# Performance work log

Measured on AMD Instinct MI355X. Metric: run time of the kernel, lower is better.

## Reference

```python
import jax, jax.numpy as jnp
import numpy as np
import math

D_MODEL = 1024
N_HEADS = 16
D_HEAD = D_MODEL // N_HEADS


def setup_inputs() -> dict:
    key = jax.random.key(0)
    ks = jax.random.split(key, 9)
    B, S = 4, 2048
    scale = 1.0 / math.sqrt(D_MODEL)
    x = jax.random.normal(ks[0], (B, S, D_MODEL), dtype=jnp.float32)
    # nn.Linear weights stored as [out, in]; we keep [in, out] for x @ W
    w_q = jax.random.uniform(ks[1], (D_MODEL, D_MODEL), jnp.float32, -scale, scale)
    b_q = jax.random.uniform(ks[2], (D_MODEL,), jnp.float32, -scale, scale)
    w_k = jax.random.uniform(ks[3], (D_MODEL, D_MODEL), jnp.float32, -scale, scale)
    b_k = jax.random.uniform(ks[4], (D_MODEL,), jnp.float32, -scale, scale)
    w_v = jax.random.uniform(ks[5], (D_MODEL, D_MODEL), jnp.float32, -scale, scale)
    b_v = jax.random.uniform(ks[6], (D_MODEL,), jnp.float32, -scale, scale)
    w_o = jax.random.uniform(ks[7], (D_MODEL, D_MODEL), jnp.float32, -scale, scale)
    b_o = jax.random.uniform(ks[8], (D_MODEL,), jnp.float32, -scale, scale)
    return {"x": x, "w_q": w_q, "b_q": b_q, "w_k": w_k, "b_k": b_k,
            "w_v": w_v, "b_v": b_v, "w_o": w_o, "b_o": b_o}


def reference(x, w_q, b_q, w_k, b_k, w_v, b_v, w_o, b_o):
    B, S, _ = x.shape
    def split_heads(t):  # [B,S,D] -> [B,H,S,Dh]
        return t.reshape(B, S, N_HEADS, D_HEAD).transpose(0, 2, 1, 3)
    q = split_heads(x @ w_q + b_q)
    k = split_heads(x @ w_k + b_k)
    v = split_heads(x @ w_v + b_v)
    scores = jnp.einsum('bhqd,bhkd->bhqk', q, k) / math.sqrt(D_HEAD)
    attn = jax.nn.softmax(scores, axis=-1)  # dropout p=0 -> identity
    ctx = jnp.einsum('bhqk,bhkd->bhqd', attn, v)
    ctx = ctx.transpose(0, 2, 1, 3).reshape(B, S, D_MODEL)
    return ctx @ w_o + b_o
```

## Files before the change

### kernel.cpp

```cpp
#include <hip/hip_runtime.h>
#include <hip/hip_bf16.h>

#define DM   1024
#define SEQ  2048
#define NH   16
#define DH   64
#define BH   64
#define MTOT 8192

typedef __attribute__((ext_vector_type(8)))  short short8;
typedef __attribute__((ext_vector_type(4)))  short short4v;
typedef __attribute__((ext_vector_type(4)))  float f32x4;
typedef __attribute__((ext_vector_type(2)))  float f32x2;
typedef __attribute__((ext_vector_type(16))) float f32x16;
typedef __attribute__((ext_vector_type(4)))  float fvec4;
typedef __attribute__((ext_vector_type(4)))  int   i32x4;
typedef unsigned short ushort_t;

#define AS1 __attribute__((address_space(1)))
#define AS3 __attribute__((address_space(3)))

#define QSCALE 0.18033688011112042f

static __device__ __forceinline__ unsigned short f2bf(float f){
  __bf16 h = (__bf16)f;
  return __builtin_bit_cast(unsigned short, h);
}

static __device__ __forceinline__ float fexp2(float x){
  float r;
  asm("v_exp_f32 %0, %1" : "=v"(r) : "v"(x));
  return r;
}

static __device__ __forceinline__ f32x2 pkadd(f32x2 a, f32x2 b){
  f32x2 d;
  asm("v_pk_add_f32 %0, %1, %2" : "=v"(d) : "v"(a), "v"(b));
  return d;
}

static __device__ __forceinline__ void gld16(const void* g, void* l){
  __builtin_amdgcn_global_load_lds((const AS1 int*)g, (AS3 int*)l, 16, 0, 0);
}

__global__ void k_cast_x(const float* __restrict__ x, ushort_t* __restrict__ xb){
  const size_t i = (size_t)blockIdx.x*256 + threadIdx.x;
  const fvec4* xv = (const fvec4*)x;
  fvec4 a = xv[2*i], b = xv[2*i+1];
  short8 r;
  #pragma unroll
  for (int j=0;j<4;++j) r[j]   = (short)f2bf(a[j]);
  #pragma unroll
  for (int j=0;j<4;++j) r[4+j] = (short)f2bf(b[j]);
  ((short8*)xb)[i] = r;
}

__global__ void k_cast_wt(const float* __restrict__ wq, const float* __restrict__ wk,
                          const float* __restrict__ wv, const float* __restrict__ wo,
                          ushort_t* __restrict__ wt){
  const int z = blockIdx.y;
  const float* W = (z==0)?wq:(z==1)?wk:(z==2)?wv:wo;
  ushort_t* Wt = wt + (size_t)z*DM*DM;
  const int k0 = (blockIdx.x & 15)*64, n0 = (blockIdx.x >> 4)*64;
  __shared__ float tile[64][65];
  const int t = threadIdx.x;
  #pragma unroll
  for (int it=0; it<4; ++it){
    int c = it*256 + t;
    int rr = c>>4, cc = c&15;
    fvec4 v = *(const fvec4*)(W + (size_t)(k0+rr)*DM + n0 + cc*4);
    #pragma unroll
    for (int j=0;j<4;++j) tile[cc*4+j][rr] = v[j];
  }
  __syncthreads();
  #pragma unroll
  for (int it=0; it<4; ++it){
    int c = it*256 + t;
    int nn = c>>4, kk = c&15;
    short4v r;
    #pragma unroll
    for (int j=0;j<4;++j) r[j] = (short)f2bf(tile[nn][kk*4+j]);
    *(short4v*)(Wt + (size_t)(n0+nn)*DM + k0 + kk*4) = r;
  }
}

template<int MODE>
__global__ __launch_bounds__(256, 2)
void k_gemm128(const ushort_t* __restrict__ A, const ushort_t* __restrict__ WtBase,
               const float* __restrict__ b0, const float* __restrict__ b1,
               const float* __restrict__ b2,
               ushort_t* __restrict__ obf, float* __restrict__ of32){
  const int by = blockIdx.y;
  const int z  = (MODE==0) ? (by>>3) : 0;
  const int n0 = (MODE==0) ? ((by&7)*128) : by*128;
  const ushort_t* Wt = WtBase + (size_t)z*DM*DM;
  const float* bias = (z==0)? b0 : (z==1? b1 : b2);
  __shared__ ushort_t Al[128*32];
  __shared__ ushort_t Bl[128*32];
  const int t = threadIdx.x;
  const int wid = t>>6, l = t&63, g = l>>4, li = l&15;
  const int m0 = blockIdx.x*128;
  const int wr = (wid>>1)*64, wc = (wid&1)*64;
  const int srow = t>>2, schunk = (t&3)*8;

  f32x4 acc[4][4] = {};

  for (int kt = 0; kt < DM; kt += 32){
    __syncthreads();
    #pragma unroll
    for (int c = 0; c < 2; ++c){
      gld16(A  + (size_t)(m0 + c*64 + srow)*DM + kt + schunk, (char*)Al + c*4096 + wid*1024);
      gld16(Wt + (size_t)(n0 + c*64 + srow)*DM + kt + schunk, (char*)Bl + c*4096 + wid*1024);
    }
    __syncthreads();
    short8 af[4], bw[4];
    #pragma unroll
    for (int mt=0; mt<4; ++mt)
      af[mt] = *(const short8*)(Al + (wr + mt*16 + li)*32 + g*8);
    #pragma unroll
    for (int nt=0; nt<4; ++nt)
      bw[nt] = *(const short8*)(Bl + (wc + nt*16 + li)*32 + g*8);
    #pragma unroll
    for (int mt=0; mt<4; ++mt)
      #pragma unroll
      for (int nt=0; nt<4; ++nt)
        acc[mt][nt] = __builtin_amdgcn_mfma_f32_16x16x32_bf16(af[mt], bw[nt], acc[mt][nt], 0,0,0);
  }

  if constexpr (MODE==0){
    if (z == 2){
      ushort_t* vt = obf + (size_t)2*MTOT*DM;
      #pragma unroll
      for (int nt=0; nt<4; ++nt){
        const int n = n0 + wc + nt*16 + li;
        const float bn = bias[n];
        const int h = n>>6, d = n&63;
        #pragma unroll
        for (int mt=0; mt<4; ++mt){
          const int m = m0 + wr + mt*16 + g*4;
          const int bb = m >> 11, s = m & 2047;
          short4v pk;
          #pragma unroll
          for (int r=0; r<4; ++r) pk[r] = (short)f2bf(acc[mt][nt][r] + bn);
          *(short4v*)(vt + (((size_t)(bb*NH + h)*DH + d)*SEQ + s)) = pk;
        }
      }
    } else {
      const float sc = (z==0) ? QSCALE : 1.f;
      #pragma unroll
      for (int nt=0; nt<4; ++nt){
        const int n = n0 + wc + nt*16 + li;
        const float bn = bias[n];
        #pragma unroll
        for (int mt=0; mt<4; ++mt){
          #pragma unroll
          for (int r=0; r<4; ++r){
            const int m = m0 + wr + mt*16 + g*4 + r;
            const float v = (acc[mt][nt][r] + bn)*sc;
            const int bb = m >> 11, s = m & 2047, h = n >> 6, d = n & 63;
            obf[(size_t)z*MTOT*DM + (((size_t)(bb*NH + h)*SEQ + s)*DH + d)] = f2bf(v);
          }
        }
      }
    }
  } else {
    #pragma unroll
    for (int nt=0; nt<4; ++nt){
      const int n = n0 + wc + nt*16 + li;
      const float bn = bias[n];
      #pragma unroll
      for (int mt=0; mt<4; ++mt){
        #pragma unroll
        for (int r=0; r<4; ++r){
          const int m = m0 + wr + mt*16 + g*4 + r;
          of32[(size_t)m*DM + n] = acc[mt][nt][r] + bn;
        }
      }
    }
  }
}

__global__ __launch_bounds__(256, 3)
void k_attn(const ushort_t* __restrict__ Qb, const ushort_t* __restrict__ Kb,
            const ushort_t* __restrict__ Vtb, ushort_t* __restrict__ ctx){
  const int swz = (blockIdx.x & 7)*128 + (blockIdx.x >> 3);
  const int qb = swz & 15, bh = swz >> 4;
  const int b = bh>>4, h = bh&15;
  const int t = threadIdx.x, wid = t>>6, lane = t&63;
  const int lq = lane&31, hi = lane>>5;
  __shared__ ushort_t Ql[8192];
  __shared__ ushort_t Kl[2][4096];
  __shared__ ushort_t Vl[2][4096];
  const ushort_t* Qh = Qb  + (size_t)bh*SEQ*DH;
  const ushort_t* Kh = Kb  + (size_t)bh*SEQ*DH;
  const ushort_t* Vh = Vtb + (size_t)bh*DH*SEQ;

  #pragma unroll
  for (int i=0; i<2; ++i){
    const int c = wid*2 + i;
    #pragma unroll
    for (int half=0; half<2; ++half)
      gld16(Qh + (size_t)(qb*128 + half*64 + lane)*DH + c*8,
            (char*)Ql + c*2048 + half*1024);
  }

  f32x16 o0 = {}, o1 = {};
  float ls = 0.f;

  #define STAGE(kv0, bi) do {                                              \
    _Pragma("unroll")                                                      \
    for (int i=0; i<2; ++i){                                               \
      const int c = wid*2 + i;                                             \
      gld16(Kh + (size_t)((kv0)+lane)*DH + c*8, (char*)&Kl[bi][0] + c*1024);\
      gld16(Vh + (size_t)lane*SEQ + (kv0) + c*8, (char*)&Vl[bi][0] + c*1024);\
    }                                                                      \
  } while(0)

  STAGE(0, 0);
  __syncthreads();

  const char* Qp = (const char*)Ql + hi*2048 + (wid*32 + lq)*16;

  int cur = 0;
  for (int t64 = 0; t64 < SEQ/64; ++t64){
    if (t64 < SEQ/64 - 1){
      if (cur) STAGE((t64+1)*64, 0); else STAGE((t64+1)*64, 1);
    }
    const char* Kb_ = (const char*)&Kl[cur][0] + hi*1024 + lq*16;
    const char* Vb_ = (const char*)&Vl[cur][0] + hi*1024 + lq*16;

    short8 qf[4];
    #pragma unroll
    for (int ks=0; ks<4; ++ks)
      qf[ks] = *(const short8*)(Qp + ks*4096);

    short8 kf[8];
    #pragma unroll
    for (int ks=0; ks<4; ++ks){
      kf[ks]   = *(const short8*)(Kb_ + ks*2048);
      kf[4+ks] = *(const short8*)(Kb_ + ks*2048 + 512);
    }
    f32x16 s0 = {}, s1 = {};
    __builtin_amdgcn_s_setprio(1);
    #pragma unroll
    for (int ks=0; ks<4; ++ks){
      s0 = __builtin_amdgcn_mfma_f32_32x32x16_bf16(kf[ks],   qf[ks], s0, 0,0,0);
      s1 = __builtin_amdgcn_mfma_f32_32x32x16_bf16(kf[4+ks], qf[ks], s1, 0,0,0);
    }
    __builtin_amdgcn_s_setprio(0);

    #pragma unroll
    for (int r=0; r<16; ++r) s0[r] = fexp2(s0[r]);
    #pragma unroll
    for (int r=0; r<16; ++r) s1[r] = fexp2(s1[r]);
    f32x2 ac = {0.f, 0.f};
    #pragma unroll
    for (int r=0; r<16; r+=4){
      f32x2 u = pkadd(f32x2{s0[r], s0[r+1]}, f32x2{s0[r+2], s0[r+3]});
      f32x2 v = pkadd(f32x2{s1[r], s1[r+1]}, f32x2{s1[r+2], s1[r+3]});
      ac = pkadd(ac, pkadd(u, v));
    }
    ls += ac[0] + ac[1];

    short8 pa[4];
    #pragma unroll
    for (int blk=0; blk<2; ++blk){
      #pragma unroll
      for (int half=0; half<2; ++half){
        i32x4 w;
        #pragma unroll
        for (int wp=0; wp<2; ++wp){
          const int base = half*8 + 2*wp;
          float a0 = blk ? s1[base]   : s0[base];
          float a1 = blk ? s1[base+1] : s0[base+1];
          float c0 = blk ? s1[base+4] : s0[base+4];
          float c1 = blk ? s1[base+5] : s0[base+5];
          int x, y;
          asm("v_cvt_pk_bf16_f32 %0, %1, %2" : "=v"(x) : "v"(a0), "v"(a1));
          asm("v_cvt_pk_bf16_f32 %0, %1, %2" : "=v"(y) : "v"(c0), "v"(c1));
          asm("v_permlane32_swap_b32 %0, %1" : "+v"(x), "+v"(y));
          w[wp] = x; w[2+wp] = y;
        }
        pa[blk*2+half] = __builtin_bit_cast(short8, w);
      }
    }

    short8 vb[8];
    #pragma unroll
    for (int ks=0; ks<4; ++ks){
      vb[ks]   = *(const short8*)(Vb_ + ks*2048);
      vb[4+ks] = *(const short8*)(Vb_ + ks*2048 + 512);
    }
    __builtin_amdgcn_s_setprio(1);
    #pragma unroll
    for (int ks=0; ks<4; ++ks){
      o0 = __builtin_amdgcn_mfma_f32_32x32x16_bf16(pa[ks], vb[ks],   o0, 0,0,0);
      o1 = __builtin_amdgcn_mfma_f32_32x32x16_bf16(pa[ks], vb[4+ks], o1, 0,0,0);
    }
    __builtin_amdgcn_s_setprio(0);

    __syncthreads();
    cur ^= 1;
  }

  ls += __shfl_xor(ls, 32);
  const float inv = 1.f / ls;
  const int qw = qb*128 + wid*32;
  #pragma unroll
  for (int r=0; r<16; ++r){
    const float iv = __shfl(inv, (r&3) + 8*(r>>2) + 4*hi);
    const int qrow = qw + (r&3) + 8*(r>>2) + 4*hi;
    ushort_t* dst = ctx + ((size_t)(b*SEQ + qrow))*DM + h*DH;
    dst[lq]    = f2bf(o0[r]*iv);
    dst[32+lq] = f2bf(o1[r]*iv);
  }
  #undef STAGE
}

extern "C" void kernel_launch(void* const* d_in, const int* in_sizes, int n_in,
                              void* d_out, int out_size, void* d_ws, size_t ws_size,
                              hipStream_t stream){
  const float* x  = (const float*)d_in[0];
  const float* wq = (const float*)d_in[1];
  const float* bq = (const float*)d_in[2];
  const float* wk = (const float*)d_in[3];
  const float* bk = (const float*)d_in[4];
  const float* wv = (const float*)d_in[5];
  const float* bv = (const float*)d_in[6];
  const float* wo = (const float*)d_in[7];
  const float* bo = (const float*)d_in[8];
  float* out = (float*)d_out;

  ushort_t* xb  = (ushort_t*)d_ws;
  ushort_t* wt  = xb  + (size_t)MTOT*DM;
  ushort_t* qkv = wt  + (size_t)4*DM*DM;
  ushort_t* ctx = qkv + (size_t)3*MTOT*DM;

  k_cast_x<<<4096, 256, 0, stream>>>(x, xb);
  k_cast_wt<<<dim3(256,4), 256, 0, stream>>>(wq, wk, wv, wo, wt);
  k_gemm128<0><<<dim3(64,24), 256, 0, stream>>>(xb, wt, bq, bk, bv, qkv, nullptr);
  k_attn<<<1024, 256, 0, stream>>>(qkv, qkv + (size_t)MTOT*DM, qkv + (size_t)2*MTOT*DM, ctx);
  k_gemm128<1><<<dim3(64,8), 256, 0, stream>>>(ctx, wt + (size_t)3*DM*DM, bo, bo, bo, nullptr, out);
}
```

Measured before the change: 279.6 us.

## Replace QKV projection GEMM with double-buffered 256x256-tile kernel

Adds a dedicated QKV projection kernel that uses 256x256 output tiles per 512-thread block. Global-to-LDS loads for the next 64-wide K slice are issued asynchronously into a second 128KB dynamic-shared-memory buffer while MFMAs run on the current one, with explicit waitcnt/barrier staging and raised wave priority around MFMA bursts. This aims to cut the per-K-step load stalls and the extra global traffic of the old 128x128, single-buffered GEMM. The trade-offs are one block per CU because of the large LDS footprint, and a 384-block grid that leaves a partial second wave. The generic GEMM is reduced to the output-projection path only.

```diff
diff --git a/kernel.cpp b/kernel.cpp
--- a/kernel.cpp
+++ b/kernel.cpp
@@ -84,6 +84,139 @@
   }
 }
 
+__global__ __launch_bounds__(512, 2)
+void k_qkv256(const ushort_t* __restrict__ A, const ushort_t* __restrict__ WtBase,
+              const float* __restrict__ bq, const float* __restrict__ bk,
+              const float* __restrict__ bv, ushort_t* __restrict__ qkv){
+  extern __shared__ char smem[];
+  const int t = threadIdx.x, wid = t>>6, lane = t&63;
+  const int g = (lane>>4)&3, li = lane&15;
+  const int wm = wid>>2, wn = wid&3;
+  const int m0 = blockIdx.x*256;
+  const int by = blockIdx.y, z = by>>2, nt0 = (by&3)*256;
+  const ushort_t* Ap = A + (size_t)m0*DM;
+  const ushort_t* Bp = WtBase + (size_t)z*DM*DM + (size_t)nt0*DM;
+  const int irb = wid>>1;
+
+  #define ISSUE(GP, LB, kh, ktt) do{                                        \
+    _Pragma("unroll")                                                       \
+    for (int j=0;j<2;++j){                                                  \
+      const int cg = (kh)*4 + ((wid*2+j)&3);                                \
+      gld16(GP + (size_t)(irb*64 + lane)*DM + (ktt)*64 + cg*8,              \
+            (LB) + cg*4096 + irb*1024);                                     \
+    }                                                                       \
+  }while(0)
+
+  const int aoff = g*4096 + (wm*128 + li)*16;
+  const int boff = g*4096 + (wn*64  + li)*16;
+
+  f32x4 acc[8][4] = {};
+
+  ISSUE(Ap, smem,         0, 0);
+  ISSUE(Bp, smem + 65536, 0, 0);
+  ISSUE(Ap, smem,         1, 0);
+  ISSUE(Bp, smem + 65536, 1, 0);
+  asm volatile("s_waitcnt vmcnt(4)" ::: "memory");
+  __builtin_amdgcn_s_barrier();
+  asm volatile("" ::: "memory");
+
+  #define MFMA16(B0v, B1v, NF0, NF1)                                        \
+    __builtin_amdgcn_s_setprio(1);                                          \
+    _Pragma("unroll")                                                       \
+    for (int mf=0;mf<8;++mf){                                               \
+      acc[mf][NF0] = __builtin_amdgcn_mfma_f32_16x16x32_bf16(a[mf], B0v, acc[mf][NF0], 0,0,0); \
+      acc[mf][NF1] = __builtin_amdgcn_mfma_f32_16x16x32_bf16(a[mf], B1v, acc[mf][NF1], 0,0,0); \
+    }                                                                       \
+    __builtin_amdgcn_s_setprio(0)
+
+  #define BARR() __builtin_amdgcn_s_barrier(); asm volatile("" ::: "memory")
+
+  for (int kt = 0; kt < 16; ++kt){
+    char* curA = smem + (kt&1)*32768;
+    char* curB = smem + 65536 + (kt&1)*32768;
+    char* nxtA = smem + ((kt+1)&1)*32768;
+    char* nxtB = smem + 65536 + ((kt+1)&1)*32768;
+    const bool more = (kt < 15);
+    short8 a[8], b0, b1;
+
+    #pragma unroll
+    for (int mf=0;mf<8;++mf) a[mf] = *(const short8*)(curA + aoff + mf*256);
+    b0 = *(const short8*)(curB + boff);
+    b1 = *(const short8*)(curB + boff + 256);
+    if (more) ISSUE(Ap, nxtA, 0, kt+1);
+    BARR();
+    MFMA16(b0, b1, 0, 1);
+    BARR();
+
+    b0 = *(const short8*)(curB + boff + 512);
+    b1 = *(const short8*)(curB + boff + 768);
+    if (more) ISSUE(Bp, nxtB, 0, kt+1);
+    BARR();
+    MFMA16(b0, b1, 2, 3);
+    if (more) { asm volatile("s_waitcnt vmcnt(4)" ::: "memory"); }
+    else      { asm volatile("s_waitcnt vmcnt(0)" ::: "memory"); }
+    BARR();
+
+    #pragma unroll
+    for (int mf=0;mf<8;++mf) a[mf] = *(const short8*)(curA + 16384 + aoff + mf*256);
+    b0 = *(const short8*)(curB + 16384 + boff);
+    b1 = *(const short8*)(curB + 16384 + boff + 256);
+    if (more) ISSUE(Ap, nxtA, 1, kt+1);
+    BARR();
+    MFMA16(b0, b1, 0, 1);
+    BARR();
+
+    b0 = *(const short8*)(curB + 16384 + boff + 512);
+    b1 = *(const short8*)(curB + 16384 + boff + 768);
+    if (more) ISSUE(Bp, nxtB, 1, kt+1);
+    BARR();
+    MFMA16(b0, b1, 2, 3);
+    if (more) { asm volatile("s_waitcnt vmcnt(4)" ::: "memory"); }
+    BARR();
+  }
+
+  const float* bias = (z==0)? bq : (z==1? bk : bv);
+  if (z == 2){
+    ushort_t* vt = qkv + (size_t)2*MTOT*DM;
+    #pragma unroll
+    for (int nf=0;nf<4;++nf){
+      const int n = nt0 + wn*64 + nf*16 + li;
+      const float bn = bias[n];
+      const int h = n>>6, d = n&63;
+      #pragma unroll
+      for (int mf=0;mf<8;++mf){
+        const int m = m0 + wm*128 + mf*16 + g*4;
+        const int bb = m>>11, s = m&2047;
+        short4v pk;
+        #pragma unroll
+        for (int r=0;r<4;++r) pk[r] = (short)f2bf(acc[mf][nf][r] + bn);
+        *(short4v*)(vt + (((size_t)(bb*NH+h)*DH + d)*SEQ + s)) = pk;
+      }
+    }
+  } else {
+    const float sc = (z==0)? QSCALE : 1.f;
+    ushort_t* dst = qkv + (size_t)z*MTOT*DM;
+    #pragma unroll
+    for (int nf=0;nf<4;++nf){
+      const int n = nt0 + wn*64 + nf*16 + li;
+      const float bn = bias[n];
+      const int h = n>>6, d = n&63;
+      #pragma unroll
+      for (int mf=0;mf<8;++mf){
+        #pragma unroll
+        for (int r=0;r<4;++r){
+          const int m = m0 + wm*128 + mf*16 + g*4 + r;
+          const int bb = m>>11, s = m&2047;
+          dst[((size_t)(bb*NH+h)*SEQ + s)*DH + d] = f2bf((acc[mf][nf][r] + bn)*sc);
+        }
+      }
+    }
+  }
+  #undef ISSUE
+  #undef MFMA16
+  #undef BARR
+}
+
 template<int MODE>
 __global__ __launch_bounds__(256, 2)
 void k_gemm128(const ushort_t* __restrict__ A, const ushort_t* __restrict__ WtBase,
@@ -91,10 +224,10 @@
                const float* __restrict__ b2,
                ushort_t* __restrict__ obf, float* __restrict__ of32){
   const int by = blockIdx.y;
-  const int z  = (MODE==0) ? (by>>3) : 0;
-  const int n0 = (MODE==0) ? ((by&7)*128) : by*128;
+  const int z  = 0;
+  const int n0 = by*128;
   const ushort_t* Wt = WtBase + (size_t)z*DM*DM;
-  const float* bias = (z==0)? b0 : (z==1? b1 : b2);
+  const float* bias = b0;
   __shared__ ushort_t Al[128*32];
   __shared__ ushort_t Bl[128*32];
   const int t = threadIdx.x;
@@ -127,54 +260,16 @@
         acc[mt][nt] = __builtin_amdgcn_mfma_f32_16x16x32_bf16(af[mt], bw[nt], acc[mt][nt], 0,0,0);
   }
 
-  if constexpr (MODE==0){
-    if (z == 2){
-      ushort_t* vt = obf + (size_t)2*MTOT*DM;
+  #pragma unroll
+  for (int nt=0; nt<4; ++nt){
+    const int n = n0 + wc + nt*16 + li;
+    const float bn = bias[n];
+    #pragma unroll
+    for (int mt=0; mt<4; ++mt){
       #pragma unroll
-      for (int nt=0; nt<4; ++nt){
-        const int n = n0 + wc + nt*16 + li;
-        const float bn = bias[n];
-        const int h = n>>6, d = n&63;
-        #pragma unroll
-        for (int mt=0; mt<4; ++mt){
-          const int m = m0 + wr + mt*16 + g*4;
-          const int bb = m >> 11, s = m & 2047;
-          short4v pk;
-          #pragma unroll
-          for (int r=0; r<4; ++r) pk[r] = (short)f2bf(acc[mt][nt][r] + bn);
-          *(short4v*)(vt + (((size_t)(bb*NH + h)*DH + d)*SEQ + s)) = pk;
-        }
-      }
-    } else {
-      const float sc = (z==0) ? QSCALE : 1.f;
-      #pragma unroll
-      for (int nt=0; nt<4; ++nt){
-        const int n = n0 + wc + nt*16 + li;
-        const float bn = bias[n];
-        #pragma unroll
-        for (int mt=0; mt<4; ++mt){
-          #pragma unroll
-          for (int r=0; r<4; ++r){
-            const int m = m0 + wr + mt*16 + g*4 + r;
-            const float v = (acc[mt][nt][r] + bn)*sc;
-            const int bb = m >> 11, s = m & 2047, h = n >> 6, d = n & 63;
-            obf[(size_t)z*MTOT*DM + (((size_t)(bb*NH + h)*SEQ + s)*DH + d)] = f2bf(v);
-          }
-        }
-      }
-    }
-  } else {
-    #pragma unroll
-    for (int nt=0; nt<4; ++nt){
-      const int n = n0 + wc + nt*16 + li;
-      const float bn = bias[n];
-      #pragma unroll
-      for (int mt=0; mt<4; ++mt){
-        #pragma unroll
-        for (int r=0; r<4; ++r){
-          const int m = m0 + wr + mt*16 + g*4 + r;
-          of32[(size_t)m*DM + n] = acc[mt][nt][r] + bn;
-        }
+      for (int r=0; r<4; ++r){
+        const int m = m0 + wr + mt*16 + g*4 + r;
+        of32[(size_t)m*DM + n] = acc[mt][nt][r] + bn;
       }
     }
   }
@@ -336,9 +431,12 @@
   ushort_t* qkv = wt  + (size_t)4*DM*DM;
   ushort_t* ctx = qkv + (size_t)3*MTOT*DM;
 
+  hipFuncSetAttribute(reinterpret_cast<const void*>(&k_qkv256),
+                      hipFuncAttributeMaxDynamicSharedMemorySize, 131072);
+
   k_cast_x<<<4096, 256, 0, stream>>>(x, xb);
   k_cast_wt<<<dim3(256,4), 256, 0, stream>>>(wq, wk, wv, wo, wt);
-  k_gemm128<0><<<dim3(64,24), 256, 0, stream>>>(xb, wt, bq, bk, bv, qkv, nullptr);
+  k_qkv256<<<dim3(32,12), 512, 131072, stream>>>(xb, wt, bq, bk, bv, qkv);
   k_attn<<<1024, 256, 0, stream>>>(qkv, qkv + (size_t)MTOT*DM, qkv + (size_t)2*MTOT*DM, ctx);
   k_gemm128<1><<<dim3(64,8), 256, 0, stream>>>(ctx, wt + (size_t)3*DM*DM, bo, bo, bo, nullptr, out);
 }
```

New measurement: 297.9 us. 6.5% more time.
